# Kernel tuning notes

Measured on AMD Instinct MI355X. Metric: run time of the kernel, lower is better.

Reference implementation:

```python
import jax, jax.numpy as jnp
import numpy as np

H, KVH, HD, D, FF = 16, 4, 128, 2048, 7168
EPS = 1e-5
ROPE_THETA = 10000.0
SCALE_FACTOR, SCALE_GAP = 1.0, 0.7


def rms_norm(x, w):
    v = jnp.mean(jnp.square(x.astype(jnp.float32)), axis=-1, keepdims=True)
    return (x.astype(jnp.float32) * jax.lax.rsqrt(v + EPS)).astype(x.dtype) * w


def apply_rope(x, pos):
    # x: [B,S,h,HD], pos: [S]
    inv = 1.0 / (ROPE_THETA ** (jnp.arange(0, HD, 2, dtype=jnp.float32) / HD))
    ang = pos.astype(jnp.float32)[:, None] * inv[None, :]              # [S,HD/2]
    cos = jnp.concatenate([jnp.cos(ang)] * 2, -1)[None, :, None, :]    # [1,S,1,HD]
    sin = jnp.concatenate([jnp.sin(ang)] * 2, -1)[None, :, None, :]
    x1, x2 = jnp.split(x, 2, axis=-1)
    rot = jnp.concatenate([-x2, x1], axis=-1)
    return x * cos + rot * sin


def attention(x, q_w, k_w, v_w, o_w):
    B, S, _ = x.shape
    pos = jnp.arange(S)
    q = apply_rope((x @ q_w.T).reshape(B, S, H, HD), pos)
    k = apply_rope((x @ k_w.T).reshape(B, S, KVH, HD), pos)
    v = (x @ v_w.T).reshape(B, S, KVH, HD)
    rep = H // KVH
    k = jnp.repeat(k, rep, axis=2)   # [B,S,H,HD]
    v = jnp.repeat(v, rep, axis=2)
    scores = jnp.einsum('bqhd,bkhd->bhqk', q, k) / np.sqrt(HD).astype(np.float32)
    causal = jnp.tril(jnp.ones((S, S), dtype=bool))
    scores = jnp.where(causal[None, None], scores, jnp.finfo(scores.dtype).min)
    probs = jax.nn.softmax(scores, axis=-1)
    out = jnp.einsum('bhqk,bkhd->bqhd', probs, v).reshape(B, S, H * HD)
    return out @ o_w.T


def mlp(x, gate_w, up_w, down_w):
    return (jax.nn.silu(x @ gate_w.T) * (x @ up_w.T)) @ down_w.T


def setup_inputs() -> dict:
    key = jax.random.key(0)
    ks = jax.random.split(key, 12)
    B, S = 2, 2048
    w = lambda k, shp: (jax.random.normal(k, shp, dtype=jnp.float32) * 0.02)
    return {
        'hidden_states': jax.random.normal(ks[0], (B, S, D), dtype=jnp.float32),
        'topk_mask': jax.random.randint(ks[1], (B, S), 0, 2) > 0,
        'topk_scores': jax.random.uniform(ks[2], (B, S), dtype=jnp.float32),
        'ln1_w': jnp.ones((D,), jnp.float32),
        'ln2_w': jnp.ones((D,), jnp.float32),
        'q_w': w(ks[3], (H * HD, D)),
        'k_w': w(ks[4], (KVH * HD, D)),
        'v_w': w(ks[5], (KVH * HD, D)),
        'o_w': w(ks[6], (D, H * HD)),
        'gate_w': w(ks[7], (FF, D)),
        'up_w': w(ks[8], (FF, D)),
        'down_w': w(ks[9], (D, FF)),
    }


def reference(hidden_states, topk_mask, topk_scores, ln1_w, ln2_w,
              q_w, k_w, v_w, o_w, gate_w, up_w, down_w):
    # attention block
    h = hidden_states + attention(rms_norm(hidden_states, ln1_w), q_w, k_w, v_w, o_w)
    # MoD top-k masked MLP: only selected tokens go through MLP, scaled, scattered back
    m = mlp(rms_norm(h, ln2_w), gate_w, up_w, down_w)
    scores = 0.5 * SCALE_FACTOR + (topk_scores - 0.5) * SCALE_GAP
    upd = jnp.where(topk_mask[..., None], m * scores[..., None], 0.0)
    return h + upd
```

## Files before the change

kernel.cpp:

```cpp
#include <hip/hip_runtime.h>
#include <stdint.h>

#define SEQ    2048
#define DMODEL 2048
#define NTOK   4096
#define NHEAD  16
#define NKVH   4
#define HDIM   128
#define FFDIM  7168
#define FFH    3584
#define QKVS   3072

typedef __bf16 bf16x8 __attribute__((ext_vector_type(8)));
typedef float  floatx4 __attribute__((ext_vector_type(4)));

__device__ __forceinline__ float bf2f(unsigned short u) {
  union { unsigned int i; float f; } v; v.i = ((unsigned int)u) << 16; return v.f;
}
__device__ __forceinline__ unsigned short f2bf(float f) {
  union { float f; unsigned int u; } v; v.f = f;
  unsigned int r = (v.u + 0x7FFFu + ((v.u >> 16) & 1u)) >> 16;
  return (unsigned short)r;
}
__device__ __forceinline__ uint4 ld8f32(const float* p) {
  float4 a = *(const float4*)p, b = *(const float4*)(p + 4);
  union { unsigned short s[8]; uint4 v; } o;
  o.s[0] = f2bf(a.x); o.s[1] = f2bf(a.y); o.s[2] = f2bf(a.z); o.s[3] = f2bf(a.w);
  o.s[4] = f2bf(b.x); o.s[5] = f2bf(b.y); o.s[6] = f2bf(b.z); o.s[7] = f2bf(b.w);
  return o.v;
}

__device__ __forceinline__ void gload16(const unsigned short* g, unsigned short* l) {
  __builtin_amdgcn_global_load_lds(
      (const __attribute__((address_space(1))) unsigned int*)g,
      (__attribute__((address_space(3))) unsigned int*)l, 16, 0, 0);
}

__global__ __launch_bounds__(256) void wconv(const float* __restrict__ s,
                                             unsigned short* __restrict__ d) {
  const size_t i = ((size_t)blockIdx.x * 256 + threadIdx.x) * 8;
  *(uint4*)(d + i) = ld8f32(s + i);
}

__global__ __launch_bounds__(256) void wconv_dn(const float* __restrict__ s,
                                                unsigned short* __restrict__ d, int koff) {
  const int r = blockIdx.x;
  const float* sp = s + (size_t)r * FFDIM + koff;
  unsigned short* dp = d + (size_t)r * FFH;
  for (int c = threadIdx.x * 8; c < FFH; c += 2048)
    *(uint4*)(dp + c) = ld8f32(sp + c);
}

#define GEMM_CORE(Aptr, Wptr, KK)                                                \
  __shared__ __align__(16) unsigned short As[128 * 32];                          \
  __shared__ __align__(16) unsigned short Bs[128 * 32];                          \
  const int tid  = threadIdx.x;                                                  \
  const int wave = tid >> 6, lane = tid & 63;                                    \
  const int quad = lane >> 4, l16 = lane & 15;                                   \
  const int row0 = blockIdx.y * 128, col0 = blockIdx.x * 128;                    \
  const int wm = (wave >> 1) * 64, wn = (wave & 1) * 64;                         \
  const floatx4 z = {0.f, 0.f, 0.f, 0.f};                                       \
  floatx4 acc[4][4];                                                             \
  _Pragma("unroll") for (int i = 0; i < 4; ++i)                                  \
  _Pragma("unroll") for (int j = 0; j < 4; ++j) acc[i][j] = z;                   \
  const int ar0 = tid >> 2, ac0 = (tid & 3) << 3;                                \
  unsigned short* lA0 = &As[wave * 512];                                         \
  unsigned short* lA1 = &As[2048 + wave * 512];                                  \
  unsigned short* lB0 = &Bs[wave * 512];                                         \
  unsigned short* lB1 = &Bs[2048 + wave * 512];                                  \
  const unsigned short* gA0 = (Aptr) + (size_t)(row0 + ar0) * (KK) + ac0;        \
  const unsigned short* gA1 = (Aptr) + (size_t)(row0 + 64 + ar0) * (KK) + ac0;   \
  const unsigned short* gB0 = (Wptr) + (size_t)(col0 + ar0) * (KK) + ac0;        \
  const unsigned short* gB1 = (Wptr) + (size_t)(col0 + 64 + ar0) * (KK) + ac0;   \
  for (int k0 = 0; k0 < (KK); k0 += 32) {                                        \
    gload16(gA0 + k0, lA0);                                                      \
    gload16(gA1 + k0, lA1);                                                      \
    gload16(gB0 + k0, lB0);                                                      \
    gload16(gB1 + k0, lB1);                                                      \
    __syncthreads();                                                             \
    bf16x8 af[4], bfr[4];                                                        \
    _Pragma("unroll") for (int i = 0; i < 4; ++i) {                              \
      af[i]  = *(const bf16x8*)&As[(wm + i * 16 + l16) * 32 + quad * 8];         \
      bfr[i] = *(const bf16x8*)&Bs[(wn + i * 16 + l16) * 32 + quad * 8];         \
    }                                                                            \
    _Pragma("unroll") for (int mi = 0; mi < 4; ++mi)                             \
    _Pragma("unroll") for (int ni = 0; ni < 4; ++ni)                             \
      acc[mi][ni] =                                                              \
          __builtin_amdgcn_mfma_f32_16x16x32_bf16(af[mi], bfr[ni], acc[mi][ni], 0, 0, 0); \
    __syncthreads();                                                             \
  }

__global__ __launch_bounds__(256) void gemm_bt(
    const unsigned short* __restrict__ A, const unsigned short* __restrict__ W,
    unsigned short* __restrict__ C, int N, int K) {
  GEMM_CORE(A, W, K)
#pragma unroll
  for (int mi = 0; mi < 4; ++mi) {
    const int r = row0 + wm + mi * 16 + quad * 4;
#pragma unroll
    for (int ni = 0; ni < 4; ++ni) {
      const int cc = col0 + wn + ni * 16 + l16;
#pragma unroll
      for (int reg = 0; reg < 4; ++reg)
        C[(size_t)(r + reg) * N + cc] = f2bf(acc[mi][ni][reg]);
    }
  }
}

__global__ __launch_bounds__(256) void gemm_o_res(
    const unsigned short* __restrict__ A, const unsigned short* __restrict__ W,
    const float* __restrict__ X, float* __restrict__ Hout) {
  GEMM_CORE(A, W, DMODEL)
#pragma unroll
  for (int mi = 0; mi < 4; ++mi) {
    const int r = row0 + wm + mi * 16 + quad * 4;
#pragma unroll
    for (int ni = 0; ni < 4; ++ni) {
      const int cc = col0 + wn + ni * 16 + l16;
#pragma unroll
      for (int reg = 0; reg < 4; ++reg) {
        const size_t idx = (size_t)(r + reg) * DMODEL + cc;
        Hout[idx] = X[idx] + acc[mi][ni][reg];
      }
    }
  }
}

__global__ __launch_bounds__(256) void gemm_down_p(
    const unsigned short* __restrict__ A, const unsigned short* __restrict__ W,
    float* __restrict__ out) {
  GEMM_CORE(A, W, FFH)
#pragma unroll
  for (int mi = 0; mi < 4; ++mi) {
    const int r = row0 + wm + mi * 16 + quad * 4;
#pragma unroll
    for (int ni = 0; ni < 4; ++ni) {
      const int cc = col0 + wn + ni * 16 + l16;
#pragma unroll
      for (int reg = 0; reg < 4; ++reg)
        out[(size_t)(r + reg) * DMODEL + cc] = acc[mi][ni][reg];
    }
  }
}

__global__ __launch_bounds__(256) void gemm_down_f(
    const unsigned short* __restrict__ A, const unsigned short* __restrict__ W,
    const float* __restrict__ H, const int* __restrict__ mask,
    const float* __restrict__ ts, float* __restrict__ out) {
  GEMM_CORE(A, W, FFH)
#pragma unroll
  for (int mi = 0; mi < 4; ++mi) {
    const int r = row0 + wm + mi * 16 + quad * 4;
#pragma unroll
    for (int ni = 0; ni < 4; ++ni) {
      const int cc = col0 + wn + ni * 16 + l16;
#pragma unroll
      for (int reg = 0; reg < 4; ++reg) {
        const int rr = r + reg;
        const size_t idx = (size_t)rr * DMODEL + cc;
        const float scv = 0.5f + (ts[rr] - 0.5f) * 0.7f;
        const float sum = out[idx] + acc[mi][ni][reg];
        out[idx] = H[idx] + (mask[rr] ? sum * scv : 0.f);
      }
    }
  }
}

__global__ __launch_bounds__(256) void gemm_gateup(
    const unsigned short* __restrict__ A, const unsigned short* __restrict__ G,
    const unsigned short* __restrict__ U, unsigned short* __restrict__ act) {
  __shared__ __align__(16) unsigned short As[128 * 32];
  __shared__ __align__(16) unsigned short Gs[64 * 32];
  __shared__ __align__(16) unsigned short Us[64 * 32];
  const int tid  = threadIdx.x;
  const int wave = tid >> 6, lane = tid & 63;
  const int quad = lane >> 4, l16 = lane & 15;
  const int row0 = blockIdx.y * 128, colg = blockIdx.x * 64;
  const int wm = (wave >> 1) * 64, wn = (wave & 1) * 32;

  const floatx4 z = {0.f, 0.f, 0.f, 0.f};
  floatx4 accG[4][2], accU[4][2];
#pragma unroll
  for (int i = 0; i < 4; ++i)
#pragma unroll
    for (int j = 0; j < 2; ++j) { accG[i][j] = z; accU[i][j] = z; }

  const int ar0 = tid >> 2, ac0 = (tid & 3) << 3;
  unsigned short* lA0 = &As[wave * 512];
  unsigned short* lA1 = &As[2048 + wave * 512];
  unsigned short* lG  = &Gs[wave * 512];
  unsigned short* lU  = &Us[wave * 512];
  const unsigned short* gA0 = A + (size_t)(row0 + ar0) * DMODEL + ac0;
  const unsigned short* gA1 = A + (size_t)(row0 + 64 + ar0) * DMODEL + ac0;
  const unsigned short* gG  = G + (size_t)(colg + ar0) * DMODEL + ac0;
  const unsigned short* gU  = U + (size_t)(colg + ar0) * DMODEL + ac0;

  for (int k0 = 0; k0 < DMODEL; k0 += 32) {
    gload16(gA0 + k0, lA0);
    gload16(gA1 + k0, lA1);
    gload16(gG + k0, lG);
    gload16(gU + k0, lU);
    __syncthreads();
    bf16x8 af[4], bg[2], bu[2];
#pragma unroll
    for (int i = 0; i < 4; ++i)
      af[i] = *(const bf16x8*)&As[(wm + i * 16 + l16) * 32 + quad * 8];
#pragma unroll
    for (int j = 0; j < 2; ++j) {
      bg[j] = *(const bf16x8*)&Gs[(wn + j * 16 + l16) * 32 + quad * 8];
      bu[j] = *(const bf16x8*)&Us[(wn + j * 16 + l16) * 32 + quad * 8];
    }
#pragma unroll
    for (int mi = 0; mi < 4; ++mi)
#pragma unroll
      for (int ni = 0; ni < 2; ++ni) {
        accG[mi][ni] = __builtin_amdgcn_mfma_f32_16x16x32_bf16(af[mi], bg[ni], accG[mi][ni], 0, 0, 0);
        accU[mi][ni] = __builtin_amdgcn_mfma_f32_16x16x32_bf16(af[mi], bu[ni], accU[mi][ni], 0, 0, 0);
      }
    __syncthreads();
  }
#pragma unroll
  for (int mi = 0; mi < 4; ++mi) {
    const int r = row0 + wm + mi * 16 + quad * 4;
#pragma unroll
    for (int ni = 0; ni < 2; ++ni) {
      const int cc = colg + wn + ni * 16 + l16;
#pragma unroll
      for (int reg = 0; reg < 4; ++reg) {
        const float g = accG[mi][ni][reg];
        const float u = accU[mi][ni][reg];
        const float s = g / (1.f + __expf(-g));
        act[(size_t)(r + reg) * FFH + cc] = f2bf(s * u);
      }
    }
  }
}

__global__ __launch_bounds__(256) void rmsnorm_f32(
    const float* __restrict__ x, const float* __restrict__ w,
    unsigned short* __restrict__ out) {
  __shared__ float red[4];
  const int row = blockIdx.x, tid = threadIdx.x;
  const int lane = tid & 63, wave = tid >> 6;
  const size_t base = (size_t)row * DMODEL + tid * 8;
  float4 a = *(const float4*)(x + base);
  float4 b = *(const float4*)(x + base + 4);
  float v[8] = {a.x, a.y, a.z, a.w, b.x, b.y, b.z, b.w};
  float ss = 0.f;
#pragma unroll
  for (int j = 0; j < 8; ++j) ss += v[j] * v[j];
#pragma unroll
  for (int off = 32; off; off >>= 1) ss += __shfl_xor(ss, off);
  if (lane == 0) red[wave] = ss;
  __syncthreads();
  const float tot = red[0] + red[1] + red[2] + red[3];
  const float rms = rsqrtf(tot * (1.f / (float)DMODEL) + 1e-5f);
  float4 wa = *(const float4*)(w + tid * 8);
  float4 wb = *(const float4*)(w + tid * 8 + 4);
  const float wv[8] = {wa.x, wa.y, wa.z, wa.w, wb.x, wb.y, wb.z, wb.w};
  unsigned short o[8];
#pragma unroll
  for (int j = 0; j < 8; ++j) o[j] = f2bf(v[j] * rms * wv[j]);
  *(uint4*)(out + base) = *(const uint4*)o;
}

__global__ __launch_bounds__(256) void rope_k(unsigned short* __restrict__ buf,
                                              int nh, int rstride) {
  const int t = blockIdx.x;
  const int s = t & (SEQ - 1);
  const int d = threadIdx.x & 63;
  const float inv = __expf((float)d * -0.14391156843712787f);
  float sn, cs;
  __sincosf((float)s * inv, &sn, &cs);
  const int npair = nh * 64;
  for (int idx = threadIdx.x; idx < npair; idx += 256) {
    const int hh = idx >> 6;
    unsigned short* p = buf + (size_t)t * rstride + hh * 128 + d;
    const float x1 = bf2f(p[0]), x2 = bf2f(p[64]);
    p[0]  = f2bf(x1 * cs - x2 * sn);
    p[64] = f2bf(x2 * cs + x1 * sn);
  }
}

__global__ __launch_bounds__(512, 4) void attn(
    const unsigned short* __restrict__ QKV,
    unsigned short* __restrict__ O) {
  __shared__ __align__(16) unsigned short Ks[64 * 136];
  __shared__ __align__(16) unsigned short Vt[128 * 80];
  __shared__ __align__(16) unsigned short Ps[8][16 * 88];
  const int h = blockIdx.x, qt = blockIdx.y, b = blockIdx.z;
  const int kvh = h >> 2;
  const int tid = threadIdx.x, wave = tid >> 6, lane = tid & 63;
  const int quad = lane >> 4, l16 = lane & 15;
  const int qbase = qt * 128;
  const int wlo = qbase + wave * 16;

  bf16x8 qf[4];
  {
    const unsigned short* qp =
        QKV + (size_t)(b * SEQ + wlo + l16) * QKVS + h * HDIM + quad * 8;
#pragma unroll
    for (int c = 0; c < 4; ++c) qf[c] = *(const bf16x8*)(qp + 32 * c);
  }
  const floatx4 z = {0.f, 0.f, 0.f, 0.f};
  floatx4 accO[8];
#pragma unroll
  for (int i = 0; i < 8; ++i) accO[i] = z;
  float mrow[4], lrow[4];
#pragma unroll
  for (int r = 0; r < 4; ++r) { mrow[r] = -1e30f; lrow[r] = 0.f; }
  const int qrowC = wlo + quad * 4;
  const float sscale = 0.08838834764831845f;

  const int sr = tid >> 4, scol = (tid & 15) * 8;
  const unsigned short* kvb = QKV + (size_t)(b * SEQ) * QKVS + kvh * HDIM;
  uint4 kreg[2], vreg[2];

  auto LOADT = [&](int t0) {
#pragma unroll
    for (int it = 0; it < 2; ++it) {
      const int r = sr + it * 32;
      kreg[it] = *(const uint4*)(kvb + (size_t)(t0 + r) * QKVS + 2048 + scol);
      vreg[it] = *(const uint4*)(kvb + (size_t)(t0 + r) * QKVS + 2560 + scol);
    }
  };
  auto STORET = [&]() {
#pragma unroll
    for (int it = 0; it < 2; ++it) {
      const int r = sr + it * 32;
      *(uint4*)&Ks[r * 136 + scol] = kreg[it];
      const unsigned short* dv = (const unsigned short*)&vreg[it];
      const int tb = r >> 3, pos = r & 7;
#pragma unroll
      for (int j = 0; j < 8; ++j) {
        const int d = scol + j;
        const int sb = tb ^ ((d >> 3) & 7);
        Vt[d * 80 + sb * 8 + pos] = dv[j];
      }
    }
  };

  const int ntiles = 2 * qt + 2;
  LOADT(0);
  STORET();
  __syncthreads();

  for (int ti = 0; ti < ntiles; ++ti) {
    const int t0 = ti * 64;
    const bool more = (ti + 1 < ntiles);
    if (more) LOADT(t0 + 64);

    const bool wskip = (t0 > wlo + 15);
    if (!wskip) {
      floatx4 sc[4];
      __builtin_amdgcn_s_setprio(1);
#pragma unroll
      for (int ni = 0; ni < 4; ++ni) {
        floatx4 s = z;
#pragma unroll
        for (int c = 0; c < 4; ++c) {
          bf16x8 kf = *(const bf16x8*)&Ks[(ni * 16 + l16) * 136 + c * 32 + quad * 8];
          s = __builtin_amdgcn_mfma_f32_16x16x32_bf16(qf[c], kf, s, 0, 0, 0);
        }
        sc[ni] = s;
      }
      __builtin_amdgcn_s_setprio(0);

      if (t0 + 63 > wlo) {
#pragma unroll
        for (int ni = 0; ni < 4; ++ni) {
          const int kcol = t0 + ni * 16 + l16;
#pragma unroll
          for (int reg = 0; reg < 4; ++reg) {
            const float vv = sc[ni][reg] * sscale;
            sc[ni][reg] = (kcol > qrowC + reg) ? -1e30f : vv;
          }
        }
      } else {
#pragma unroll
        for (int ni = 0; ni < 4; ++ni)
#pragma unroll
          for (int reg = 0; reg < 4; ++reg) sc[ni][reg] *= sscale;
      }

      float mx[4];
#pragma unroll
      for (int reg = 0; reg < 4; ++reg) {
        float m0 = fmaxf(fmaxf(sc[0][reg], sc[1][reg]), fmaxf(sc[2][reg], sc[3][reg]));
#pragma unroll
        for (int off = 1; off < 16; off <<= 1) m0 = fmaxf(m0, __shfl_xor(m0, off));
        mx[reg] = m0;
      }
      const bool grow = (mx[0] > mrow[0] + 8.f) || (mx[1] > mrow[1] + 8.f) ||
                        (mx[2] > mrow[2] + 8.f) || (mx[3] > mrow[3] + 8.f);
      if (__any(grow)) {
#pragma unroll
        for (int reg = 0; reg < 4; ++reg) {
          const float mnew = fmaxf(mrow[reg], mx[reg]);
          const float alpha = __expf(mrow[reg] - mnew);
          mrow[reg] = mnew;
          lrow[reg] *= alpha;
#pragma unroll
          for (int nd = 0; nd < 8; ++nd) accO[nd][reg] *= alpha;
        }
      }
#pragma unroll
      for (int reg = 0; reg < 4; ++reg) {
        float rs = 0.f;
#pragma unroll
        for (int ni = 0; ni < 4; ++ni) {
          const float p = __expf(sc[ni][reg] - mrow[reg]);
          sc[ni][reg] = p;
          rs += p;
        }
#pragma unroll
        for (int off = 1; off < 16; off <<= 1) rs += __shfl_xor(rs, off);
        lrow[reg] += rs;
      }
#pragma unroll
      for (int ni = 0; ni < 4; ++ni)
#pragma unroll
        for (int reg = 0; reg < 4; ++reg)
          Ps[wave][(quad * 4 + reg) * 88 + ni * 16 + l16] = f2bf(sc[ni][reg]);
      const bf16x8 pa0 = *(const bf16x8*)&Ps[wave][l16 * 88 + quad * 8];
      const bf16x8 pa1 = *(const bf16x8*)&Ps[wave][l16 * 88 + 32 + quad * 8];
      __builtin_amdgcn_s_setprio(1);
#pragma unroll
      for (int nd = 0; nd < 8; ++nd) {
        const int d = nd * 16 + l16;
        const int f = (d >> 3) & 7;
        bf16x8 v0 = *(const bf16x8*)&Vt[d * 80 + ((quad ^ f) << 3)];
        bf16x8 v1 = *(const bf16x8*)&Vt[d * 80 + (((quad + 4) ^ f) << 3)];
        accO[nd] = __builtin_amdgcn_mfma_f32_16x16x32_bf16(pa0, v0, accO[nd], 0, 0, 0);
        accO[nd] = __builtin_amdgcn_mfma_f32_16x16x32_bf16(pa1, v1, accO[nd], 0, 0, 0);
      }
      __builtin_amdgcn_s_setprio(0);
    }
    __syncthreads();
    if (more) {
      STORET();
      __syncthreads();
    }
  }
#pragma unroll
  for (int nd = 0; nd < 8; ++nd)
#pragma unroll
    for (int reg = 0; reg < 4; ++reg) {
      const float o = accO[nd][reg] / lrow[reg];
      O[(size_t)(b * SEQ + qrowC + reg) * (NHEAD * HDIM) + h * HDIM + nd * 16 + l16] = f2bf(o);
    }
}

extern "C" void kernel_launch(void* const* d_in, const int* in_sizes, int n_in,
                              void* d_out, int out_size, void* d_ws, size_t ws_size,
                              hipStream_t stream) {
  (void)in_sizes; (void)n_in; (void)out_size; (void)ws_size;
  const float* x    = (const float*)d_in[0];
  const int*   mask = (const int*)d_in[1];
  const float* ts   = (const float*)d_in[2];
  const float* ln1  = (const float*)d_in[3];
  const float* ln2  = (const float*)d_in[4];
  const float* q_w  = (const float*)d_in[5];
  const float* k_w  = (const float*)d_in[6];
  const float* v_w  = (const float*)d_in[7];
  const float* o_w  = (const float*)d_in[8];
  const float* g_w  = (const float*)d_in[9];
  const float* u_w  = (const float*)d_in[10];
  const float* dn_w = (const float*)d_in[11];
  float* out = (float*)d_out;

  char* ws = (char*)d_ws;
  unsigned short* xn    = (unsigned short*)(ws + 0);
  unsigned short* qkv   = (unsigned short*)(ws + 16777216);
  unsigned short* wqkv  = (unsigned short*)(ws + 41943040);
  unsigned short* attno = (unsigned short*)(ws + 41943040);
  unsigned short* wo    = (unsigned short*)(ws + 58720256);
  unsigned short* wg    = (unsigned short*)(ws + 16777216);
  unsigned short* wu    = (unsigned short*)(ws + 31457280);
  unsigned short* wdn   = (unsigned short*)(ws + 16777216);
  unsigned short* act   = (unsigned short*)(ws + 46137344);
  float*          hbuf  = (float*)         (ws + 75497472);

  wconv<<<2048, 256, 0, stream>>>(q_w, wqkv);
  wconv<<<512,  256, 0, stream>>>(k_w, wqkv + (size_t)2048 * DMODEL);
  wconv<<<512,  256, 0, stream>>>(v_w, wqkv + (size_t)2560 * DMODEL);
  wconv<<<2048, 256, 0, stream>>>(o_w, wo);

  rmsnorm_f32<<<NTOK, 256, 0, stream>>>(x, ln1, xn);
  gemm_bt<<<dim3(QKVS / 128, 32), 256, 0, stream>>>(xn, wqkv, qkv, QKVS, 2048);
  rope_k<<<NTOK, 256, 0, stream>>>(qkv, 20, QKVS);
  attn<<<dim3(NHEAD, SEQ / 128, 2), 512, 0, stream>>>(qkv, attno);
  gemm_o_res<<<dim3(16, 32), 256, 0, stream>>>(attno, wo, x, hbuf);

  rmsnorm_f32<<<NTOK, 256, 0, stream>>>(hbuf, ln2, xn);
  for (int hf = 0; hf < 2; ++hf) {
    wconv<<<3584, 256, 0, stream>>>(g_w + (size_t)hf * FFH * DMODEL, wg);
    wconv<<<3584, 256, 0, stream>>>(u_w + (size_t)hf * FFH * DMODEL, wu);
    gemm_gateup<<<dim3(FFH / 64, 32), 256, 0, stream>>>(xn, wg, wu, act);
    wconv_dn<<<2048, 256, 0, stream>>>(dn_w, wdn, hf * FFH);
    if (hf == 0)
      gemm_down_p<<<dim3(16, 32), 256, 0, stream>>>(act, wdn, out);
    else
      gemm_down_f<<<dim3(16, 32), 256, 0, stream>>>(act, wdn, hbuf, mask, ts, out);
  }
}
```

Measured before the change: 1.088 ms.

## Gather masked tokens for the MLP and pair causal attention query tiles

The MLP now runs only on tokens whose mask is set. An atomic-counter gather compacts their normalized rows, the gate/up and down GEMM blocks past the count exit early, and the down GEMM scatters scaled results into the output in place, which removes the separate hbuf residual buffer. The attention kernel now gives each block one low and one high causal query tile (qt and 15-qt) so per-block work is balanced, and halves the grid. This adds atomics, nondeterministic token order, and more register pressure in attention, which is why the launch-bounds occupancy hint is lowered.

```diff
diff --git a/kernel.cpp b/kernel.cpp
--- a/kernel.cpp
+++ b/kernel.cpp
@@ -126,9 +126,12 @@
   }
 }
 
-__global__ __launch_bounds__(256) void gemm_down_p(
+__global__ __launch_bounds__(256) void gemm_down_add(
     const unsigned short* __restrict__ A, const unsigned short* __restrict__ W,
-    float* __restrict__ out) {
+    const float* __restrict__ ts, const int* __restrict__ tok_of,
+    const int* __restrict__ cnt, float* __restrict__ out) {
+  const int nrow = *cnt;
+  if (blockIdx.y * 128 >= nrow) return;
   GEMM_CORE(A, W, FFH)
 #pragma unroll
   for (int mi = 0; mi < 4; ++mi) {
@@ -137,30 +140,13 @@
     for (int ni = 0; ni < 4; ++ni) {
       const int cc = col0 + wn + ni * 16 + l16;
 #pragma unroll
-      for (int reg = 0; reg < 4; ++reg)
-        out[(size_t)(r + reg) * DMODEL + cc] = acc[mi][ni][reg];
-    }
-  }
-}
-
-__global__ __launch_bounds__(256) void gemm_down_f(
-    const unsigned short* __restrict__ A, const unsigned short* __restrict__ W,
-    const float* __restrict__ H, const int* __restrict__ mask,
-    const float* __restrict__ ts, float* __restrict__ out) {
-  GEMM_CORE(A, W, FFH)
-#pragma unroll
-  for (int mi = 0; mi < 4; ++mi) {
-    const int r = row0 + wm + mi * 16 + quad * 4;
-#pragma unroll
-    for (int ni = 0; ni < 4; ++ni) {
-      const int cc = col0 + wn + ni * 16 + l16;
-#pragma unroll
       for (int reg = 0; reg < 4; ++reg) {
         const int rr = r + reg;
-        const size_t idx = (size_t)rr * DMODEL + cc;
-        const float scv = 0.5f + (ts[rr] - 0.5f) * 0.7f;
-        const float sum = out[idx] + acc[mi][ni][reg];
-        out[idx] = H[idx] + (mask[rr] ? sum * scv : 0.f);
+        if (rr < nrow) {
+          const int tok = tok_of[rr];
+          const float scv = 0.5f + (ts[tok] - 0.5f) * 0.7f;
+          out[(size_t)tok * DMODEL + cc] += acc[mi][ni][reg] * scv;
+        }
       }
     }
   }
@@ -168,7 +154,9 @@
 
 __global__ __launch_bounds__(256) void gemm_gateup(
     const unsigned short* __restrict__ A, const unsigned short* __restrict__ G,
-    const unsigned short* __restrict__ U, unsigned short* __restrict__ act) {
+    const unsigned short* __restrict__ U, const int* __restrict__ cnt,
+    unsigned short* __restrict__ act) {
+  if (blockIdx.y * 128 >= *cnt) return;
   __shared__ __align__(16) unsigned short As[128 * 32];
   __shared__ __align__(16) unsigned short Gs[64 * 32];
   __shared__ __align__(16) unsigned short Us[64 * 32];
@@ -262,6 +250,40 @@
 #pragma unroll
   for (int j = 0; j < 8; ++j) o[j] = f2bf(v[j] * rms * wv[j]);
   *(uint4*)(out + base) = *(const uint4*)o;
+}
+
+__global__ void zero_cnt(int* cnt) { *cnt = 0; }
+
+__global__ __launch_bounds__(256) void rms_gather(
+    const float* __restrict__ x, const float* __restrict__ w,
+    const int* __restrict__ mask, int* __restrict__ cnt,
+    int* __restrict__ tok_of, unsigned short* __restrict__ xc) {
+  const int row = blockIdx.x;
+  if (!mask[row]) return;
+  __shared__ float red[4];
+  __shared__ int ppos;
+  const int tid = threadIdx.x, lane = tid & 63, wave = tid >> 6;
+  if (tid == 0) { const int p = atomicAdd(cnt, 1); ppos = p; tok_of[p] = row; }
+  const size_t base = (size_t)row * DMODEL + tid * 8;
+  float4 a = *(const float4*)(x + base);
+  float4 b = *(const float4*)(x + base + 4);
+  float v[8] = {a.x, a.y, a.z, a.w, b.x, b.y, b.z, b.w};
+  float ss = 0.f;
+#pragma unroll
+  for (int j = 0; j < 8; ++j) ss += v[j] * v[j];
+#pragma unroll
+  for (int off = 32; off; off >>= 1) ss += __shfl_xor(ss, off);
+  if (lane == 0) red[wave] = ss;
+  __syncthreads();
+  const float tot = red[0] + red[1] + red[2] + red[3];
+  const float rms = rsqrtf(tot * (1.f / (float)DMODEL) + 1e-5f);
+  float4 wa = *(const float4*)(w + tid * 8);
+  float4 wb = *(const float4*)(w + tid * 8 + 4);
+  const float wv[8] = {wa.x, wa.y, wa.z, wa.w, wb.x, wb.y, wb.z, wb.w};
+  unsigned short o[8];
+#pragma unroll
+  for (int j = 0; j < 8; ++j) o[j] = f2bf(v[j] * rms * wv[j]);
+  *(uint4*)(xc + (size_t)ppos * DMODEL + tid * 8) = *(const uint4*)o;
 }
 
 __global__ __launch_bounds__(256) void rope_k(unsigned short* __restrict__ buf,
@@ -282,35 +304,41 @@
   }
 }
 
-__global__ __launch_bounds__(512, 4) void attn(
+__global__ __launch_bounds__(512, 2) void attn(
     const unsigned short* __restrict__ QKV,
     unsigned short* __restrict__ O) {
   __shared__ __align__(16) unsigned short Ks[64 * 136];
   __shared__ __align__(16) unsigned short Vt[128 * 80];
   __shared__ __align__(16) unsigned short Ps[8][16 * 88];
-  const int h = blockIdx.x, qt = blockIdx.y, b = blockIdx.z;
+  const int h = blockIdx.x, b = blockIdx.z;
+  const int qtL = blockIdx.y, qtH = 15 - qtL;
   const int kvh = h >> 2;
   const int tid = threadIdx.x, wave = tid >> 6, lane = tid & 63;
   const int quad = lane >> 4, l16 = lane & 15;
-  const int qbase = qt * 128;
-  const int wlo = qbase + wave * 16;
-
-  bf16x8 qf[4];
+  const int wloH = qtH * 128 + wave * 16;
+  const int wloL = qtL * 128 + wave * 16;
+  const int qrH = wloH + quad * 4, qrL = wloL + quad * 4;
+  const float sscale = 0.08838834764831845f;
+
+  bf16x8 qfH[4], qfL[4];
   {
-    const unsigned short* qp =
-        QKV + (size_t)(b * SEQ + wlo + l16) * QKVS + h * HDIM + quad * 8;
-#pragma unroll
-    for (int c = 0; c < 4; ++c) qf[c] = *(const bf16x8*)(qp + 32 * c);
+    const unsigned short* qpH =
+        QKV + (size_t)(b * SEQ + wloH + l16) * QKVS + h * HDIM + quad * 8;
+    const unsigned short* qpL =
+        QKV + (size_t)(b * SEQ + wloL + l16) * QKVS + h * HDIM + quad * 8;
+#pragma unroll
+    for (int c = 0; c < 4; ++c) {
+      qfH[c] = *(const bf16x8*)(qpH + 32 * c);
+      qfL[c] = *(const bf16x8*)(qpL + 32 * c);
+    }
   }
   const floatx4 z = {0.f, 0.f, 0.f, 0.f};
-  floatx4 accO[8];
-#pragma unroll
-  for (int i = 0; i < 8; ++i) accO[i] = z;
-  float mrow[4], lrow[4];
-#pragma unroll
-  for (int r = 0; r < 4; ++r) { mrow[r] = -1e30f; lrow[r] = 0.f; }
-  const int qrowC = wlo + quad * 4;
-  const float sscale = 0.08838834764831845f;
+  floatx4 accH[8], accL[8];
+#pragma unroll
+  for (int i = 0; i < 8; ++i) { accH[i] = z; accL[i] = z; }
+  float mH[4], lH[4], mL[4], lL[4];
+#pragma unroll
+  for (int r = 0; r < 4; ++r) { mH[r] = -1e30f; lH[r] = 0.f; mL[r] = -1e30f; lL[r] = 0.f; }
 
   const int sr = tid >> 4, scol = (tid & 15) * 8;
   const unsigned short* kvb = QKV + (size_t)(b * SEQ) * QKVS + kvh * HDIM;
@@ -340,102 +368,106 @@
     }
   };
 
-  const int ntiles = 2 * qt + 2;
+  auto COMPUTE = [&](const bf16x8* qf, floatx4* accO, float* mrow, float* lrow,
+                     int qrowC, int wlo, int t0) {
+    floatx4 sc[4];
+    __builtin_amdgcn_s_setprio(1);
+#pragma unroll
+    for (int ni = 0; ni < 4; ++ni) {
+      floatx4 s = z;
+#pragma unroll
+      for (int c = 0; c < 4; ++c) {
+        bf16x8 kf = *(const bf16x8*)&Ks[(ni * 16 + l16) * 136 + c * 32 + quad * 8];
+        s = __builtin_amdgcn_mfma_f32_16x16x32_bf16(qf[c], kf, s, 0, 0, 0);
+      }
+      sc[ni] = s;
+    }
+    __builtin_amdgcn_s_setprio(0);
+
+    if (t0 + 63 > wlo) {
+#pragma unroll
+      for (int ni = 0; ni < 4; ++ni) {
+        const int kcol = t0 + ni * 16 + l16;
+#pragma unroll
+        for (int reg = 0; reg < 4; ++reg) {
+          const float vv = sc[ni][reg] * sscale;
+          sc[ni][reg] = (kcol > qrowC + reg) ? -1e30f : vv;
+        }
+      }
+    } else {
+#pragma unroll
+      for (int ni = 0; ni < 4; ++ni)
+#pragma unroll
+        for (int reg = 0; reg < 4; ++reg) sc[ni][reg] *= sscale;
+    }
+
+    float mx[4];
+#pragma unroll
+    for (int reg = 0; reg < 4; ++reg) {
+      float m0 = fmaxf(fmaxf(sc[0][reg], sc[1][reg]), fmaxf(sc[2][reg], sc[3][reg]));
+#pragma unroll
+      for (int off = 1; off < 16; off <<= 1) m0 = fmaxf(m0, __shfl_xor(m0, off));
+      mx[reg] = m0;
+    }
+    const bool grow = (mx[0] > mrow[0] + 8.f) || (mx[1] > mrow[1] + 8.f) ||
+                      (mx[2] > mrow[2] + 8.f) || (mx[3] > mrow[3] + 8.f);
+    if (__any(grow)) {
+#pragma unroll
+      for (int reg = 0; reg < 4; ++reg) {
+        const float mnew = fmaxf(mrow[reg], mx[reg]);
+        const float alpha = __expf(mrow[reg] - mnew);
+        mrow[reg] = mnew;
+        lrow[reg] *= alpha;
+#pragma unroll
+        for (int nd = 0; nd < 8; ++nd) accO[nd][reg] *= alpha;
+      }
+    }
+#pragma unroll
+    for (int reg = 0; reg < 4; ++reg) {
+      float rs = 0.f;
+#pragma unroll
+      for (int ni = 0; ni < 4; ++ni) {
+        const float p = __expf(sc[ni][reg] - mrow[reg]);
+        sc[ni][reg] = p;
+        rs += p;
+      }
+#pragma unroll
+      for (int off = 1; off < 16; off <<= 1) rs += __shfl_xor(rs, off);
+      lrow[reg] += rs;
+    }
+#pragma unroll
+    for (int ni = 0; ni < 4; ++ni)
+#pragma unroll
+      for (int reg = 0; reg < 4; ++reg)
+        Ps[wave][(quad * 4 + reg) * 88 + ni * 16 + l16] = f2bf(sc[ni][reg]);
+    const bf16x8 pa0 = *(const bf16x8*)&Ps[wave][l16 * 88 + quad * 8];
+    const bf16x8 pa1 = *(const bf16x8*)&Ps[wave][l16 * 88 + 32 + quad * 8];
+    __builtin_amdgcn_s_setprio(1);
+#pragma unroll
+    for (int nd = 0; nd < 8; ++nd) {
+      const int d = nd * 16 + l16;
+      const int f = (d >> 3) & 7;
+      bf16x8 v0 = *(const bf16x8*)&Vt[d * 80 + ((quad ^ f) << 3)];
+      bf16x8 v1 = *(const bf16x8*)&Vt[d * 80 + (((quad + 4) ^ f) << 3)];
+      accO[nd] = __builtin_amdgcn_mfma_f32_16x16x32_bf16(pa0, v0, accO[nd], 0, 0, 0);
+      accO[nd] = __builtin_amdgcn_mfma_f32_16x16x32_bf16(pa1, v1, accO[nd], 0, 0, 0);
+    }
+    __builtin_amdgcn_s_setprio(0);
+  };
+
+  const int ntL = 2 * qtL + 2, ntH = 2 * qtH + 2;
   LOADT(0);
   STORET();
   __syncthreads();
 
-  for (int ti = 0; ti < ntiles; ++ti) {
+  for (int ti = 0; ti < ntH; ++ti) {
     const int t0 = ti * 64;
-    const bool more = (ti + 1 < ntiles);
+    const bool more = (ti + 1 < ntH);
     if (more) LOADT(t0 + 64);
 
-    const bool wskip = (t0 > wlo + 15);
-    if (!wskip) {
-      floatx4 sc[4];
-      __builtin_amdgcn_s_setprio(1);
-#pragma unroll
-      for (int ni = 0; ni < 4; ++ni) {
-        floatx4 s = z;
-#pragma unroll
-        for (int c = 0; c < 4; ++c) {
-          bf16x8 kf = *(const bf16x8*)&Ks[(ni * 16 + l16) * 136 + c * 32 + quad * 8];
-          s = __builtin_amdgcn_mfma_f32_16x16x32_bf16(qf[c], kf, s, 0, 0, 0);
-        }
-        sc[ni] = s;
-      }
-      __builtin_amdgcn_s_setprio(0);
-
-      if (t0 + 63 > wlo) {
-#pragma unroll
-        for (int ni = 0; ni < 4; ++ni) {
-          const int kcol = t0 + ni * 16 + l16;
-#pragma unroll
-          for (int reg = 0; reg < 4; ++reg) {
-            const float vv = sc[ni][reg] * sscale;
-            sc[ni][reg] = (kcol > qrowC + reg) ? -1e30f : vv;
-          }
-        }
-      } else {
-#pragma unroll
-        for (int ni = 0; ni < 4; ++ni)
-#pragma unroll
-          for (int reg = 0; reg < 4; ++reg) sc[ni][reg] *= sscale;
-      }
-
-      float mx[4];
-#pragma unroll
-      for (int reg = 0; reg < 4; ++reg) {
-        float m0 = fmaxf(fmaxf(sc[0][reg], sc[1][reg]), fmaxf(sc[2][reg], sc[3][reg]));
-#pragma unroll
-        for (int off = 1; off < 16; off <<= 1) m0 = fmaxf(m0, __shfl_xor(m0, off));
-        mx[reg] = m0;
-      }
-      const bool grow = (mx[0] > mrow[0] + 8.f) || (mx[1] > mrow[1] + 8.f) ||
-                        (mx[2] > mrow[2] + 8.f) || (mx[3] > mrow[3] + 8.f);
-      if (__any(grow)) {
-#pragma unroll
-        for (int reg = 0; reg < 4; ++reg) {
-          const float mnew = fmaxf(mrow[reg], mx[reg]);
-          const float alpha = __expf(mrow[reg] - mnew);
-          mrow[reg] = mnew;
-          lrow[reg] *= alpha;
-#pragma unroll
-          for (int nd = 0; nd < 8; ++nd) accO[nd][reg] *= alpha;
-        }
-      }
-#pragma unroll
-      for (int reg = 0; reg < 4; ++reg) {
-        float rs = 0.f;
-#pragma unroll
-        for (int ni = 0; ni < 4; ++ni) {
-          const float p = __expf(sc[ni][reg] - mrow[reg]);
-          sc[ni][reg] = p;
-          rs += p;
-        }
-#pragma unroll
-        for (int off = 1; off < 16; off <<= 1) rs += __shfl_xor(rs, off);
-        lrow[reg] += rs;
-      }
-#pragma unroll
-      for (int ni = 0; ni < 4; ++ni)
-#pragma unroll
-        for (int reg = 0; reg < 4; ++reg)
-          Ps[wave][(quad * 4 + reg) * 88 + ni * 16 + l16] = f2bf(sc[ni][reg]);
-      const bf16x8 pa0 = *(const bf16x8*)&Ps[wave][l16 * 88 + quad * 8];
-      const bf16x8 pa1 = *(const bf16x8*)&Ps[wave][l16 * 88 + 32 + quad * 8];
-      __builtin_amdgcn_s_setprio(1);
-#pragma unroll
-      for (int nd = 0; nd < 8; ++nd) {
-        const int d = nd * 16 + l16;
-        const int f = (d >> 3) & 7;
-        bf16x8 v0 = *(const bf16x8*)&Vt[d * 80 + ((quad ^ f) << 3)];
-        bf16x8 v1 = *(const bf16x8*)&Vt[d * 80 + (((quad + 4) ^ f) << 3)];
-        accO[nd] = __builtin_amdgcn_mfma_f32_16x16x32_bf16(pa0, v0, accO[nd], 0, 0, 0);
-        accO[nd] = __builtin_amdgcn_mfma_f32_16x16x32_bf16(pa1, v1, accO[nd], 0, 0, 0);
-      }
-      __builtin_amdgcn_s_setprio(0);
-    }
+    if (t0 <= wloH + 15) COMPUTE(qfH, accH, mH, lH, qrH, wloH, t0);
+    if (ti < ntL && t0 <= wloL + 15) COMPUTE(qfL, accL, mL, lL, qrL, wloL, t0);
+
     __syncthreads();
     if (more) {
       STORET();
@@ -446,8 +478,10 @@
   for (int nd = 0; nd < 8; ++nd)
 #pragma unroll
     for (int reg = 0; reg < 4; ++reg) {
-      const float o = accO[nd][reg] / lrow[reg];
-      O[(size_t)(b * SEQ + qrowC + reg) * (NHEAD * HDIM) + h * HDIM + nd * 16 + l16] = f2bf(o);
+      const float oH = accH[nd][reg] / lH[reg];
+      O[(size_t)(b * SEQ + qrH + reg) * (NHEAD * HDIM) + h * HDIM + nd * 16 + l16] = f2bf(oH);
+      const float oL = accL[nd][reg] / lL[reg];
+      O[(size_t)(b * SEQ + qrL + reg) * (NHEAD * HDIM) + h * HDIM + nd * 16 + l16] = f2bf(oL);
     }
 }
 
@@ -475,11 +509,13 @@
   unsigned short* wqkv  = (unsigned short*)(ws + 41943040);
   unsigned short* attno = (unsigned short*)(ws + 41943040);
   unsigned short* wo    = (unsigned short*)(ws + 58720256);
+  unsigned short* xc    = (unsigned short*)(ws + 0);
   unsigned short* wg    = (unsigned short*)(ws + 16777216);
   unsigned short* wu    = (unsigned short*)(ws + 31457280);
   unsigned short* wdn   = (unsigned short*)(ws + 16777216);
   unsigned short* act   = (unsigned short*)(ws + 46137344);
-  float*          hbuf  = (float*)         (ws + 75497472);
+  int*            cnt   = (int*)           (ws + 75497472);
+  int*            tok_of= (int*)           (ws + 75501568);
 
   wconv<<<2048, 256, 0, stream>>>(q_w, wqkv);
   wconv<<<512,  256, 0, stream>>>(k_w, wqkv + (size_t)2048 * DMODEL);
@@ -489,18 +525,16 @@
   rmsnorm_f32<<<NTOK, 256, 0, stream>>>(x, ln1, xn);
   gemm_bt<<<dim3(QKVS / 128, 32), 256, 0, stream>>>(xn, wqkv, qkv, QKVS, 2048);
   rope_k<<<NTOK, 256, 0, stream>>>(qkv, 20, QKVS);
-  attn<<<dim3(NHEAD, SEQ / 128, 2), 512, 0, stream>>>(qkv, attno);
-  gemm_o_res<<<dim3(16, 32), 256, 0, stream>>>(attno, wo, x, hbuf);
-
-  rmsnorm_f32<<<NTOK, 256, 0, stream>>>(hbuf, ln2, xn);
+  attn<<<dim3(NHEAD, 8, 2), 512, 0, stream>>>(qkv, attno);
+  gemm_o_res<<<dim3(16, 32), 256, 0, stream>>>(attno, wo, x, out);
+
+  zero_cnt<<<1, 1, 0, stream>>>(cnt);
+  rms_gather<<<NTOK, 256, 0, stream>>>(out, ln2, mask, cnt, tok_of, xc);
   for (int hf = 0; hf < 2; ++hf) {
     wconv<<<3584, 256, 0, stream>>>(g_w + (size_t)hf * FFH * DMODEL, wg);
     wconv<<<3584, 256, 0, stream>>>(u_w + (size_t)hf * FFH * DMODEL, wu);
-    gemm_gateup<<<dim3(FFH / 64, 32), 256, 0, stream>>>(xn, wg, wu, act);
+    gemm_gateup<<<dim3(FFH / 64, 32), 256, 0, stream>>>(xc, wg, wu, cnt, act);
     wconv_dn<<<2048, 256, 0, stream>>>(dn_w, wdn, hf * FFH);
-    if (hf == 0)
-      gemm_down_p<<<dim3(16, 32), 256, 0, stream>>>(act, wdn, out);
-    else
-      gemm_down_f<<<dim3(16, 32), 256, 0, stream>>>(act, wdn, hbuf, mask, ts, out);
-  }
-}
+    gemm_down_add<<<dim3(16, 32), 256, 0, stream>>>(act, wdn, ts, tok_of, cnt, out);
+  }
+}
```

Measured after the change: 942.0 us. -13.4%, faster.
